# Optimization experiments

Hardware: AMD Instinct MI355X
Metric: run time of the kernel (lower is better)

Reference implementation:

```python
import jax, jax.numpy as jnp
import numpy as np

NUM_HEADS = 4   # forced by reshape(B, N, num_heads, C) of a dim*4 projection
BN_EPS = 1e-5


def _chamfer(a, b):
    # a, b: [B, N, 3] -> symmetric chamfer distance (mean of nearest sq-dists)
    d = (jnp.sum(a ** 2, -1)[:, :, None] + jnp.sum(b ** 2, -1)[:, None, :]
         - 2.0 * jnp.einsum('bnc,bmc->bnm', a, b))
    return jnp.mean(jnp.min(d, axis=2)) + jnp.mean(jnp.min(d, axis=1))


def _forward(xs, pc1, bn_gamma, bn_beta, q_w, kv_w, proj_w, proj_b, map_w, map_b):
    B, F, C, N = xs.shape
    H = NUM_HEADS
    scale = C ** -0.5  # head_dim == dim in this module (full-dim heads)

    def per_item(x):  # x: [F, C, N]
        # BatchNorm1d in eval mode (running_mean=0, running_var=1)
        xn = (x / jnp.sqrt(1.0 + BN_EPS)) * bn_gamma[:, None] + bn_beta[:, None]
        xn = xn.transpose(0, 2, 1)                 # [F, N, C]
        xr = xn[::-1]                              # flip over frame axis
        q = (xn @ q_w.T).reshape(F, N, H, C).transpose(0, 2, 1, 3)        # [F,H,N,C]
        kv = (xr @ kv_w.T).reshape(F, N, 2, H, C).transpose(2, 0, 3, 1, 4)
        k, v = kv[0], kv[1]                        # [F,H,N,C]
        attn = jax.nn.softmax(jnp.einsum('fhnc,fhmc->fhnm', q, k) * scale, axis=-1)
        o = jnp.einsum('fhnm,fhmc->fhnc', attn, v).transpose(0, 2, 1, 3)  # [F,N,H,C]
        xa = (o[0] + o[1]).transpose(1, 0, 2)      # [H, N, C]: sum of first two frames
        xa = xa @ proj_w.T + proj_b                # [H, N, C] x_appearance
        fr = xa @ map_w.T + map_b                  # [H, N, 3] frames (mapping_xyz)
        return xa, fr

    xa, frames = jax.vmap(per_item)(xs)            # [B,H,N,C], [B,H,N,3]
    pc1t = pc1.transpose(0, 2, 1)                  # [B, N, 3]
    loss = _chamfer(pc1t + frames[:, 0], pc1t)
    return xa[:, 1:], frames[:, 1:], loss


def setup_inputs() -> dict:
    key = jax.random.key(0)
    ks = jax.random.split(key, 8)
    B, F, C, N = 2, 4, 64, 2048
    return {
        'xs': jax.random.normal(ks[0], (B, F, C, N), jnp.float32),
        'pc1': jax.random.normal(ks[1], (B, 3, N), jnp.float32),
        'pc2': jax.random.normal(ks[2], (B, 3, N), jnp.float32),
        'bn_gamma': jnp.ones((C,), jnp.float32),
        'bn_beta': jnp.zeros((C,), jnp.float32),
        'q_w': 0.02 * jax.random.normal(ks[3], (4 * C, C), jnp.float32),
        'kv_w': 0.02 * jax.random.normal(ks[4], (8 * C, C), jnp.float32),
        'proj_w': 0.02 * jax.random.normal(ks[5], (C, C), jnp.float32),
        'proj_b': jnp.zeros((C,), jnp.float32),
        'map_w': 0.02 * jax.random.normal(ks[6], (3, C), jnp.float32),
        'map_b': jnp.zeros((3,), jnp.float32),
    }


def reference(xs, pc1, pc2, bn_gamma, bn_beta, q_w, kv_w, proj_w, proj_b, map_w, map_b):
    # pc2 is accepted by the torch forward but unused in its body
    return _forward(xs, pc1, bn_gamma, bn_beta, q_w, kv_w, proj_w, proj_b, map_w, map_b)
```

## Files before the change

### kernel.cpp

```cpp
#include <hip/hip_runtime.h>
#include <hip/hip_bf16.h>

#define NPTS 2048
#define LOG2E 1.4426950408889634f
#define NJC 16
#define JCH 128
#define KSPLIT 8

typedef short bf16x8 __attribute__((ext_vector_type(8)));
typedef float f32x4 __attribute__((ext_vector_type(4)));
typedef unsigned uint32x4 __attribute__((ext_vector_type(4)));
typedef __attribute__((address_space(3))) char lds_char;
typedef __attribute__((address_space(1))) const char glob_char;

union PBU { uint32x4 u; bf16x8 v; };

static __device__ __forceinline__ unsigned cvt_pk_bf16(float a, float b) {
    unsigned r;
    asm("v_cvt_pk_bf16_f32 %0, %1, %2" : "=v"(r) : "v"(a), "v"(b));
    return r;
}
static __device__ __forceinline__ float b2f(unsigned short u) {
    return __uint_as_float((unsigned)u << 16);
}

__global__ __launch_bounds__(256) void prep_all(const float* __restrict__ xs,
                                                const float* __restrict__ gamma,
                                                const float* __restrict__ beta,
                                                const float* __restrict__ q_w,
                                                const float* __restrict__ kv_w,
                                                const float* __restrict__ proj_w,
                                                __hip_bfloat16* __restrict__ xT,
                                                __hip_bfloat16* __restrict__ Wpb,
                                                __hip_bfloat16* __restrict__ Wb) {
    const int bid = blockIdx.x;
    const int t = threadIdx.x;
    if (bid < 256) {
        const int fr = bid >> 5;
        const int n0 = (bid & 31) * 64;
        const float* __restrict__ A = xs + (size_t)fr * 64 * NPTS;

        __shared__ float As[64][68];
        __shared__ float sg[64], sb[64];

        if (t < 64) {
            const float inv = 1.0f / sqrtf(1.0f + 1e-5f);
            sg[t] = gamma[t] * inv;
            sb[t] = beta[t];
        }
        const int tx = t & 15, ty = t >> 4;
        for (int r = 0; r < 4; ++r) {
            int row = ty + 16 * r, col = tx * 4;
            *(float4*)&As[row][col] = *(const float4*)&A[(size_t)row * NPTS + n0 + col];
        }
        __syncthreads();

        const int nl = t >> 2, c0 = (t & 3) * 16;
        bf16x8 v0, v1;
#pragma unroll
        for (int j = 0; j < 8; ++j) {
            float a = As[c0 + j][nl] * sg[c0 + j] + sb[c0 + j];
            v0[j] = (short)__bfloat16_as_ushort(__float2bfloat16(a));
        }
#pragma unroll
        for (int j = 0; j < 8; ++j) {
            float a = As[c0 + 8 + j][nl] * sg[c0 + 8 + j] + sb[c0 + 8 + j];
            v1[j] = (short)__bfloat16_as_ushort(__float2bfloat16(a));
        }
        __hip_bfloat16* dst = xT + ((size_t)fr * NPTS + n0 + nl) * 64 + c0;
        *(bf16x8*)(dst) = v0;
        *(bf16x8*)(dst + 8) = v1;
    } else {
        const int row = (bid - 256) * 256 + t;
        if (row < 768) {
            const float* src;
            float scale;
            if (row < 256) { src = q_w + row * 64;          scale = 0.125f * LOG2E; }
            else           { src = kv_w + (row - 256) * 64; scale = 1.0f; }
            for (int c = 0; c < 64; ++c)
                Wpb[row * 64 + c] = __float2bfloat16(src[c] * scale);
        } else if (row < 832) {
            const int j = row - 768;
            for (int c = 0; c < 64; ++c)
                Wb[j * 64 + c] = __float2bfloat16(proj_w[j * 64 + c]);
        }
    }
}

__global__ __launch_bounds__(256) void qkv_mfma(const __hip_bfloat16* __restrict__ xT,
                                                const __hip_bfloat16* __restrict__ Wpb,
                                                __hip_bfloat16* __restrict__ Qg,
                                                __hip_bfloat16* __restrict__ Kg,
                                                __hip_bfloat16* __restrict__ Vtg) {
    const int bf = blockIdx.z;
    const int b = bf >> 1, f01 = bf & 1;
    const int jt = blockIdx.y;
    const int f_src = (jt < 4) ? f01 : (3 - f01);
    const int n0 = blockIdx.x * 64;

    const int t = threadIdx.x, lane = t & 63, w = t >> 6;
    const int l15 = lane & 15, g = (lane >> 4) & 3;

    const __hip_bfloat16* __restrict__ xfb = xT + (size_t)(b * 4 + f_src) * NPTS * 64;

    if (jt < 8) {
        const __hip_bfloat16* wp = Wpb + (size_t)(jt * 64 + w * 16 + l15) * 64 + g * 8;
        bf16x8 wf0 = *(const bf16x8*)(wp);
        bf16x8 wf1 = *(const bf16x8*)(wp + 32);
        __hip_bfloat16* __restrict__ dst = (jt < 4 ? Qg : Kg) + (size_t)bf * NPTS * 256;
        const int jb = (jt & 3) * 64 + w * 16 + g * 4;
#pragma unroll
        for (int nt = 0; nt < 4; ++nt) {
            const __hip_bfloat16* xp = xfb + (size_t)(n0 + nt * 16 + l15) * 64 + g * 8;
            bf16x8 xf0 = *(const bf16x8*)(xp);
            bf16x8 xf1 = *(const bf16x8*)(xp + 32);
            f32x4 d = (f32x4){0.f, 0.f, 0.f, 0.f};
            d = __builtin_amdgcn_mfma_f32_16x16x32_bf16(wf0, xf0, d, 0, 0, 0);
            d = __builtin_amdgcn_mfma_f32_16x16x32_bf16(wf1, xf1, d, 0, 0, 0);
            uint2 pv;
            pv.x = cvt_pk_bf16(d[0], d[1]);
            pv.y = cvt_pk_bf16(d[2], d[3]);
            *(uint2*)&dst[(size_t)(n0 + nt * 16 + l15) * 256 + jb] = pv;
        }
    } else {
        const __hip_bfloat16* xp = xfb + (size_t)(n0 + w * 16 + l15) * 64 + g * 8;
        bf16x8 xf0 = *(const bf16x8*)(xp);
        bf16x8 xf1 = *(const bf16x8*)(xp + 32);
        __hip_bfloat16* __restrict__ dst = Vtg + (size_t)bf * 256 * NPTS;
#pragma unroll
        for (int tj = 0; tj < 4; ++tj) {
            const int ch = (jt - 8) * 64 + tj * 16 + l15;
            const __hip_bfloat16* wp = Wpb + (size_t)(512 + ch) * 64 + g * 8;
            bf16x8 wf0 = *(const bf16x8*)(wp);
            bf16x8 wf1 = *(const bf16x8*)(wp + 32);
            f32x4 d = (f32x4){0.f, 0.f, 0.f, 0.f};
            d = __builtin_amdgcn_mfma_f32_16x16x32_bf16(xf0, wf0, d, 0, 0, 0);
            d = __builtin_amdgcn_mfma_f32_16x16x32_bf16(xf1, wf1, d, 0, 0, 0);
            uint2 pv;
            pv.x = cvt_pk_bf16(d[0], d[1]);
            pv.y = cvt_pk_bf16(d[2], d[3]);
            *(uint2*)&dst[(size_t)ch * NPTS + n0 + w * 16 + g * 4] = pv;
        }
    }
}

__global__ __launch_bounds__(256, 4) void attn_mfma(const __hip_bfloat16* __restrict__ Qg,
                                                    const __hip_bfloat16* __restrict__ Kg,
                                                    const __hip_bfloat16* __restrict__ Vtg,
                                                    __hip_bfloat16* __restrict__ OTb,
                                                    float* __restrict__ Lp) {
    const int combo = blockIdx.x;
    const int bf = combo >> 2, h = combo & 3;
    const int n0 = blockIdx.y * 128;
    const int split = blockIdx.z;
    const int kbase = split * (NPTS / KSPLIT);
    const int NT = NPTS / KSPLIT / 32;

    __shared__ __align__(16) char smem[32768];

    const int t = threadIdx.x;
    const int lane = t & 63, w = t >> 6;
    const int l15 = lane & 15, g = (lane >> 4) & 3;

    const int krow = w * 8 + (lane >> 3), kslot = lane & 7;
    const int vrow = w * 16 + (lane >> 2), vslot = lane & 3;
    const int kcs = (kslot ^ (krow & 7)) * 8;
    const int vcs = (vslot ^ ((vrow >> 1) & 3)) * 8;

    const __hip_bfloat16* qbase =
        Qg + ((size_t)bf * NPTS + n0 + w * 32 + l15) * 256 + h * 64 + g * 8;
    bf16x8 qf[2][2];
    qf[0][0] = *(const bf16x8*)(qbase);
    qf[0][1] = *(const bf16x8*)(qbase + 32);
    qf[1][0] = *(const bf16x8*)(qbase + 16 * 256);
    qf[1][1] = *(const bf16x8*)(qbase + 16 * 256 + 32);

    const __hip_bfloat16* kgb = Kg + (size_t)bf * NPTS * 256 + h * 64;
    const __hip_bfloat16* vgb = Vtg + ((size_t)bf * 256 + h * 64) * NPTS;

    int koff[2][2], voff[4];
#pragma unroll
    for (int tt = 0; tt < 2; ++tt) {
        const int row = tt * 16 + l15;
#pragma unroll
        for (int s = 0; s < 2; ++s)
            koff[tt][s] = row * 128 + (((s * 4 + g) ^ (row & 7)) << 4);
    }
#pragma unroll
    for (int ct = 0; ct < 4; ++ct) {
        const int row = ct * 16 + l15;
        voff[ct] = 4096 + row * 64 + ((g ^ ((row >> 1) & 3)) << 4);
    }

    f32x4 oacc[2][4];
    float lsum[2] = {0.f, 0.f};
#pragma unroll
    for (int f = 0; f < 2; ++f)
#pragma unroll
        for (int r = 0; r < 4; ++r) oacc[f][r] = (f32x4){0.f, 0.f, 0.f, 0.f};

    auto stage = [&](int kt) {
        const int bsel = kt & 3;
        const __hip_bfloat16* ksrc = kgb + (size_t)(kbase + kt * 32 + krow) * 256 + kcs;
        __builtin_amdgcn_global_load_lds((const glob_char*)ksrc,
            (lds_char*)(smem + bsel * 8192 + w * 1024), 16, 0, 0);
        const __hip_bfloat16* vsrc = vgb + (size_t)vrow * NPTS + kbase + kt * 32 + vcs;
        __builtin_amdgcn_global_load_lds((const glob_char*)vsrc,
            (lds_char*)(smem + bsel * 8192 + 4096 + w * 1024), 16, 0, 0);
    };

    auto tile = [&](int kt) {
        const char* B = smem + (kt & 3) * 8192;
        bf16x8 kf[2][2];
#pragma unroll
        for (int tt = 0; tt < 2; ++tt)
#pragma unroll
            for (int s = 0; s < 2; ++s)
                kf[tt][s] = *(const bf16x8*)(B + koff[tt][s]);

        bf16x8 pb[2];
#pragma unroll
        for (int f = 0; f < 2; ++f) {
            f32x4 st0 = (f32x4){0.f, 0.f, 0.f, 0.f}, st1 = st0;
            st0 = __builtin_amdgcn_mfma_f32_16x16x32_bf16(kf[0][0], qf[f][0], st0, 0, 0, 0);
            st0 = __builtin_amdgcn_mfma_f32_16x16x32_bf16(kf[0][1], qf[f][1], st0, 0, 0, 0);
            st1 = __builtin_amdgcn_mfma_f32_16x16x32_bf16(kf[1][0], qf[f][0], st1, 0, 0, 0);
            st1 = __builtin_amdgcn_mfma_f32_16x16x32_bf16(kf[1][1], qf[f][1], st1, 0, 0, 0);
            float p00 = exp2f(st0[0]);
            float p01 = exp2f(st0[1]);
            float p02 = exp2f(st0[2]);
            float p03 = exp2f(st0[3]);
            float p10 = exp2f(st1[0]);
            float p11 = exp2f(st1[1]);
            float p12 = exp2f(st1[2]);
            float p13 = exp2f(st1[3]);
            lsum[f] += ((p00 + p01) + (p02 + p03)) + ((p10 + p11) + (p12 + p13));
            unsigned x0 = cvt_pk_bf16(p00, p01);
            unsigned x1 = cvt_pk_bf16(p02, p03);
            unsigned y0 = cvt_pk_bf16(p10, p11);
            unsigned y1 = cvt_pk_bf16(p12, p13);
            asm("v_permlane32_swap_b32 %0, %1" : "+v"(x0), "+v"(y0));
            asm("v_permlane16_swap_b32 %0, %1" : "+v"(x0), "+v"(y0));
            asm("v_permlane32_swap_b32 %0, %1" : "+v"(x1), "+v"(y1));
            asm("v_permlane16_swap_b32 %0, %1" : "+v"(x1), "+v"(y1));
            PBU pu;
            pu.u = (uint32x4){x0, x1, y0, y1};
            pb[f] = pu.v;
        }

#pragma unroll
        for (int ct = 0; ct < 4; ++ct) {
            bf16x8 vf = *(const bf16x8*)(B + voff[ct]);
            oacc[0][ct] = __builtin_amdgcn_mfma_f32_16x16x32_bf16(vf, pb[0], oacc[0][ct], 0, 0, 0);
            oacc[1][ct] = __builtin_amdgcn_mfma_f32_16x16x32_bf16(vf, pb[1], oacc[1][ct], 0, 0, 0);
        }
    };

    stage(0);
    stage(1);
    for (int kt = 0; kt < NT - 2; ++kt) {
        stage(kt + 2);
        asm volatile("s_waitcnt vmcnt(4)" ::: "memory");
        asm volatile("s_waitcnt lgkmcnt(0)" ::: "memory");
        __builtin_amdgcn_s_barrier();
        asm volatile("" ::: "memory");
        tile(kt);
    }
    asm volatile("s_waitcnt vmcnt(2)" ::: "memory");
    asm volatile("s_waitcnt lgkmcnt(0)" ::: "memory");
    __builtin_amdgcn_s_barrier();
    asm volatile("" ::: "memory");
    tile(NT - 2);
    asm volatile("s_waitcnt vmcnt(0)" ::: "memory");
    asm volatile("s_waitcnt lgkmcnt(0)" ::: "memory");
    __builtin_amdgcn_s_barrier();
    asm volatile("" ::: "memory");
    tile(NT - 1);

    float l0 = lsum[0], l1 = lsum[1];
    l0 += __shfl_xor(l0, 16);
    l0 += __shfl_xor(l0, 32);
    l1 += __shfl_xor(l1, 16);
    l1 += __shfl_xor(l1, 32);
    const int qq = n0 + w * 32 + l15;
    if (lane < 16) {
        Lp[(size_t)(split * 16 + combo) * NPTS + qq] = l0;
        Lp[(size_t)(split * 16 + combo) * NPTS + qq + 16] = l1;
    }

    __hip_bfloat16* __restrict__ Op = OTb + (size_t)(split * 16 + combo) * 64 * NPTS;
#pragma unroll
    for (int ct = 0; ct < 4; ++ct)
#pragma unroll
        for (int r = 0; r < 4; ++r) {
            Op[(size_t)(ct * 16 + g * 4 + r) * NPTS + qq] = __float2bfloat16(oacc[0][ct][r]);
            Op[(size_t)(ct * 16 + g * 4 + r) * NPTS + qq + 16] = __float2bfloat16(oacc[1][ct][r]);
        }
}

__global__ __launch_bounds__(256) void proj_frames(const __hip_bfloat16* __restrict__ OTb,
                                                   const float* __restrict__ Lp,
                                                   const __hip_bfloat16* __restrict__ Wb,
                                                   const float* __restrict__ proj_b,
                                                   const float* __restrict__ map_w,
                                                   const float* __restrict__ map_b,
                                                   float* __restrict__ out,
                                                   float* __restrict__ frames0) {
    const int bh = blockIdx.y, b = bh >> 2, h = bh & 3;
    const int n0 = blockIdx.x * 64;
    const int cf0 = (b * 2 + 0) * 4 + h;
    const int cf1 = (b * 2 + 1) * 4 + h;

    __shared__ __align__(16) unsigned short Xn[64][72];
    __shared__ float xaS[64][68];

    const int t = threadIdx.x;
    const int lane = t & 63, w = t >> 6;
    const int tx = t & 15, ty = t >> 4;
    const int l15 = lane & 15, g = (lane >> 4) & 3;
    const int nc = n0 + tx * 4;

    float4 L0 = make_float4(0.f, 0.f, 0.f, 0.f), L1 = L0;
#pragma unroll
    for (int s = 0; s < KSPLIT; ++s) {
        float4 a = *(const float4*)&Lp[(size_t)(s * 16 + cf0) * NPTS + nc];
        L0.x += a.x; L0.y += a.y; L0.z += a.z; L0.w += a.w;
        float4 c = *(const float4*)&Lp[(size_t)(s * 16 + cf1) * NPTS + nc];
        L1.x += c.x; L1.y += c.y; L1.z += c.z; L1.w += c.w;
    }
    float4 inv0 = make_float4(1.f / L0.x, 1.f / L0.y, 1.f / L0.z, 1.f / L0.w);
    float4 inv1 = make_float4(1.f / L1.x, 1.f / L1.y, 1.f / L1.z, 1.f / L1.w);

    for (int r = 0; r < 4; ++r) {
        int row = ty + 16 * r, col = tx * 4;
        float x0 = 0.f, x1 = 0.f, x2 = 0.f, x3 = 0.f;
        float y0 = 0.f, y1 = 0.f, y2 = 0.f, y3 = 0.f;
#pragma unroll
        for (int s = 0; s < KSPLIT; ++s) {
            ushort4 u0 = *(const ushort4*)&OTb[((size_t)(s * 16 + cf0) * 64 + row) * NPTS + n0 + col];
            ushort4 u1 = *(const ushort4*)&OTb[((size_t)(s * 16 + cf1) * 64 + row) * NPTS + n0 + col];
            x0 += b2f(u0.x); x1 += b2f(u0.y); x2 += b2f(u0.z); x3 += b2f(u0.w);
            y0 += b2f(u1.x); y1 += b2f(u1.y); y2 += b2f(u1.z); y3 += b2f(u1.w);
        }
        Xn[col + 0][row] = __bfloat16_as_ushort(__float2bfloat16(x0 * inv0.x + y0 * inv1.x));
        Xn[col + 1][row] = __bfloat16_as_ushort(__float2bfloat16(x1 * inv0.y + y1 * inv1.y));
        Xn[col + 2][row] = __bfloat16_as_ushort(__float2bfloat16(x2 * inv0.z + y2 * inv1.z));
        Xn[col + 3][row] = __bfloat16_as_ushort(__float2bfloat16(x3 * inv0.w + y3 * inv1.w));
    }
    __syncthreads();

    {
        const __hip_bfloat16* wp = Wb + (size_t)(w * 16 + l15) * 64 + g * 8;
        bf16x8 wf0 = *(const bf16x8*)(wp);
        bf16x8 wf1 = *(const bf16x8*)(wp + 32);
        float pbias[4];
#pragma unroll
        for (int r = 0; r < 4; ++r) pbias[r] = proj_b[w * 16 + g * 4 + r];
#pragma unroll
        for (int nt = 0; nt < 4; ++nt) {
            bf16x8 xf0 = *(const bf16x8*)&Xn[nt * 16 + l15][g * 8];
            bf16x8 xf1 = *(const bf16x8*)&Xn[nt * 16 + l15][g * 8 + 32];
            f32x4 d = (f32x4){0.f, 0.f, 0.f, 0.f};
            d = __builtin_amdgcn_mfma_f32_16x16x32_bf16(wf0, xf0, d, 0, 0, 0);
            d = __builtin_amdgcn_mfma_f32_16x16x32_bf16(wf1, xf1, d, 0, 0, 0);
            float4 v = make_float4(d[0] + pbias[0], d[1] + pbias[1],
                                   d[2] + pbias[2], d[3] + pbias[3]);
            *(float4*)&xaS[nt * 16 + l15][w * 16 + g * 4] = v;
        }
    }
    __syncthreads();

    if (h >= 1) {
        float* __restrict__ xa_out = out + (size_t)(b * 3 + h - 1) * NPTS * 64;
        for (int r = 0; r < 4; ++r) {
            int n = ty + 16 * r;
            float4 v = *(const float4*)&xaS[n][tx * 4];
            *(float4*)&xa_out[(size_t)(n0 + n) * 64 + tx * 4] = v;
        }
    }

    if (t < 192) {
        int r = t / 3, j = t % 3;
        float s = map_b[j];
        for (int c = 0; c < 64; ++c) s += xaS[r][c] * map_w[j * 64 + c];
        int n = n0 + r;
        if (h == 0) frames0[((size_t)b * NPTS + n) * 3 + j] = s;
        else        out[786432 + ((size_t)(b * 3 + h - 1) * NPTS + n) * 3 + j] = s;
    }
}

__global__ __launch_bounds__(256) void chamfer_partial(const float* __restrict__ pc1,
                                                       const float* __restrict__ frames0,
                                                       float* __restrict__ partial) {
    const int z = blockIdx.z;
    const int dir = z >> 1, b = z & 1;
    const int i = blockIdx.x * 256 + threadIdx.x;
    const int j0 = blockIdx.y * JCH;
    const float* __restrict__ px = pc1 + (size_t)b * 3 * NPTS;
    const float* __restrict__ fr = frames0 + (size_t)b * NPTS * 3;

    __shared__ float4 sj[JCH];
    if (threadIdx.x < JCH) {
        int jj = j0 + threadIdx.x;
        float bx = px[jj], by = px[NPTS + jj], bz = px[2 * NPTS + jj];
        if (dir == 1) { bx += fr[jj * 3]; by += fr[jj * 3 + 1]; bz += fr[jj * 3 + 2]; }
        sj[threadIdx.x] = make_float4(bx, by, bz, bx * bx + by * by + bz * bz);
    }
    float ax = px[i], ay = px[NPTS + i], az = px[2 * NPTS + i];
    if (dir == 0) { ax += fr[i * 3]; ay += fr[i * 3 + 1]; az += fr[i * 3 + 2]; }
    const float a2 = ax * ax + ay * ay + az * az;
    __syncthreads();

    float best = 1e30f;
#pragma unroll 4
    for (int k = 0; k < JCH; ++k) {
        float4 p = sj[k];
        float d = a2 + p.w - 2.0f * (ax * p.x + ay * p.y + az * p.z);
        best = fminf(best, d);
    }
    partial[((size_t)z * NJC + blockIdx.y) * NPTS + i] = best;
}

__global__ __launch_bounds__(256) void chamfer_minsum(const float* __restrict__ partial,
                                                      double* __restrict__ sums) {
    const int gid = blockIdx.x * 256 + threadIdx.x;
    const int z = gid >> 11, i = gid & 2047;
    float best = 1e30f;
#pragma unroll
    for (int c = 0; c < NJC; ++c)
        best = fminf(best, partial[((size_t)z * NJC + c) * NPTS + i]);
    __shared__ double sm[256];
    sm[threadIdx.x] = (double)best;
    __syncthreads();
    for (int off = 128; off > 0; off >>= 1) {
        if (threadIdx.x < off) sm[threadIdx.x] += sm[threadIdx.x + off];
        __syncthreads();
    }
    if (threadIdx.x == 0) sums[blockIdx.x] = sm[0];
}

__global__ void chamfer_final(const double* __restrict__ sums, float* __restrict__ loss_out) {
    if (threadIdx.x == 0) {
        double s = 0.0;
        for (int k = 0; k < 32; ++k) s += sums[k];
        loss_out[0] = (float)(s / 4096.0);
    }
}

extern "C" void kernel_launch(void* const* d_in, const int* in_sizes, int n_in,
                              void* d_out, int out_size, void* d_ws, size_t ws_size,
                              hipStream_t stream) {
    const float* xs     = (const float*)d_in[0];
    const float* pc1    = (const float*)d_in[1];
    const float* gamma  = (const float*)d_in[3];
    const float* beta   = (const float*)d_in[4];
    const float* q_w    = (const float*)d_in[5];
    const float* kv_w   = (const float*)d_in[6];
    const float* proj_w = (const float*)d_in[7];
    const float* proj_b = (const float*)d_in[8];
    const float* map_w  = (const float*)d_in[9];
    const float* map_b  = (const float*)d_in[10];
    float* out = (float*)d_out;

    char* ws = (char*)d_ws;
    __hip_bfloat16* Qg  = (__hip_bfloat16*)(ws);
    __hip_bfloat16* Kg  = (__hip_bfloat16*)(ws + 4194304);
    __hip_bfloat16* Vtg = (__hip_bfloat16*)(ws + 8388608);
    __hip_bfloat16* OTb = (__hip_bfloat16*)(ws + 12582912);
    __hip_bfloat16* Wpb = (__hip_bfloat16*)(ws + 46137344);
    __hip_bfloat16* xT  = (__hip_bfloat16*)(ws + 46235648);
    float* frames0 = (float*)(ws + 48332800);
    float* partial = (float*)(ws + 48381952);
    double* sums   = (double*)(ws + 48906240);
    float* Lp      = (float*)(ws + 48906496);
    __hip_bfloat16* Wb  = (__hip_bfloat16*)(ws + 49955072);

    hipLaunchKernelGGL(prep_all, dim3(260), dim3(256), 0, stream,
                       xs, gamma, beta, q_w, kv_w, proj_w, xT, Wpb, Wb);
    hipLaunchKernelGGL(qkv_mfma, dim3(32, 12, 4), dim3(256), 0, stream,
                       xT, Wpb, Qg, Kg, Vtg);
    hipLaunchKernelGGL(attn_mfma, dim3(16, 16, KSPLIT), dim3(256), 0, stream,
                       Qg, Kg, Vtg, OTb, Lp);
    hipLaunchKernelGGL(proj_frames, dim3(32, 8), dim3(256), 0, stream,
                       OTb, Lp, Wb, proj_b, map_w, map_b, out, frames0);
    hipLaunchKernelGGL(chamfer_partial, dim3(NPTS / 256, NJC, 4), dim3(256), 0, stream,
                       pc1, frames0, partial);
    hipLaunchKernelGGL(chamfer_minsum, dim3(32), dim3(256), 0, stream,
                       partial, sums);
    hipLaunchKernelGGL(chamfer_final, dim3(1), dim3(64), 0, stream,
                       sums, out + 823296);
}
```

Measured before the change: 75.06 us.

## Fuse chamfer final reduction via atomic counter, add MFMA priority, drop lgkm waits

Removes the single-thread chamfer_final launch by having the last block of chamfer_minsum perform the final sum, using an atomic counter that prep_all resets. The attention kernel raises wave priority around MFMA groups with s_setprio. It also drops the explicit lgkmcnt(0) waits before the barriers in the attention pipeline. Removing those waits relies on the global_load_lds staging being covered by vmcnt alone, which could risk reading LDS data that has not landed yet.

```diff
diff --git a/kernel.cpp b/kernel.cpp
--- a/kernel.cpp
+++ b/kernel.cpp
@@ -32,7 +32,8 @@
                                                 const float* __restrict__ proj_w,
                                                 __hip_bfloat16* __restrict__ xT,
                                                 __hip_bfloat16* __restrict__ Wpb,
-                                                __hip_bfloat16* __restrict__ Wb) {
+                                                __hip_bfloat16* __restrict__ Wb,
+                                                unsigned* __restrict__ counter) {
     const int bid = blockIdx.x;
     const int t = threadIdx.x;
     if (bid < 256) {
@@ -83,6 +84,8 @@
             const int j = row - 768;
             for (int c = 0; c < 64; ++c)
                 Wb[j * 64 + c] = __float2bfloat16(proj_w[j * 64 + c]);
+        } else if (row == 1023) {
+            *counter = 0;
         }
     }
 }
@@ -222,10 +225,12 @@
 #pragma unroll
         for (int f = 0; f < 2; ++f) {
             f32x4 st0 = (f32x4){0.f, 0.f, 0.f, 0.f}, st1 = st0;
+            __builtin_amdgcn_s_setprio(1);
             st0 = __builtin_amdgcn_mfma_f32_16x16x32_bf16(kf[0][0], qf[f][0], st0, 0, 0, 0);
             st0 = __builtin_amdgcn_mfma_f32_16x16x32_bf16(kf[0][1], qf[f][1], st0, 0, 0, 0);
             st1 = __builtin_amdgcn_mfma_f32_16x16x32_bf16(kf[1][0], qf[f][0], st1, 0, 0, 0);
             st1 = __builtin_amdgcn_mfma_f32_16x16x32_bf16(kf[1][1], qf[f][1], st1, 0, 0, 0);
+            __builtin_amdgcn_s_setprio(0);
             float p00 = exp2f(st0[0]);
             float p01 = exp2f(st0[1]);
             float p02 = exp2f(st0[2]);
@@ -248,12 +253,14 @@
             pb[f] = pu.v;
         }
 
+        __builtin_amdgcn_s_setprio(1);
 #pragma unroll
         for (int ct = 0; ct < 4; ++ct) {
             bf16x8 vf = *(const bf16x8*)(B + voff[ct]);
             oacc[0][ct] = __builtin_amdgcn_mfma_f32_16x16x32_bf16(vf, pb[0], oacc[0][ct], 0, 0, 0);
             oacc[1][ct] = __builtin_amdgcn_mfma_f32_16x16x32_bf16(vf, pb[1], oacc[1][ct], 0, 0, 0);
         }
+        __builtin_amdgcn_s_setprio(0);
     };
 
     stage(0);
@@ -261,18 +268,15 @@
     for (int kt = 0; kt < NT - 2; ++kt) {
         stage(kt + 2);
         asm volatile("s_waitcnt vmcnt(4)" ::: "memory");
-        asm volatile("s_waitcnt lgkmcnt(0)" ::: "memory");
         __builtin_amdgcn_s_barrier();
         asm volatile("" ::: "memory");
         tile(kt);
     }
     asm volatile("s_waitcnt vmcnt(2)" ::: "memory");
-    asm volatile("s_waitcnt lgkmcnt(0)" ::: "memory");
     __builtin_amdgcn_s_barrier();
     asm volatile("" ::: "memory");
     tile(NT - 2);
     asm volatile("s_waitcnt vmcnt(0)" ::: "memory");
-    asm volatile("s_waitcnt lgkmcnt(0)" ::: "memory");
     __builtin_amdgcn_s_barrier();
     asm volatile("" ::: "memory");
     tile(NT - 1);
@@ -422,7 +426,9 @@
 }
 
 __global__ __launch_bounds__(256) void chamfer_minsum(const float* __restrict__ partial,
-                                                      double* __restrict__ sums) {
+                                                      double* __restrict__ sums,
+                                                      unsigned* __restrict__ counter,
+                                                      float* __restrict__ loss_out) {
     const int gid = blockIdx.x * 256 + threadIdx.x;
     const int z = gid >> 11, i = gid & 2047;
     float best = 1e30f;
@@ -436,14 +442,17 @@
         if (threadIdx.x < off) sm[threadIdx.x] += sm[threadIdx.x + off];
         __syncthreads();
     }
-    if (threadIdx.x == 0) sums[blockIdx.x] = sm[0];
-}
-
-__global__ void chamfer_final(const double* __restrict__ sums, float* __restrict__ loss_out) {
     if (threadIdx.x == 0) {
-        double s = 0.0;
-        for (int k = 0; k < 32; ++k) s += sums[k];
-        loss_out[0] = (float)(s / 4096.0);
+        sums[blockIdx.x] = sm[0];
+        __threadfence();
+        unsigned prev = atomicAdd(counter, 1u);
+        if (prev == 31u) {
+            __threadfence();
+            double s = 0.0;
+            for (int k = 0; k < 32; ++k) s += sums[k];
+            loss_out[0] = (float)(s / 4096.0);
+            *counter = 0;
+        }
     }
 }
 
@@ -474,9 +483,10 @@
     double* sums   = (double*)(ws + 48906240);
     float* Lp      = (float*)(ws + 48906496);
     __hip_bfloat16* Wb  = (__hip_bfloat16*)(ws + 49955072);
+    unsigned* counter   = (unsigned*)(ws + 49963264);
 
     hipLaunchKernelGGL(prep_all, dim3(260), dim3(256), 0, stream,
-                       xs, gamma, beta, q_w, kv_w, proj_w, xT, Wpb, Wb);
+                       xs, gamma, beta, q_w, kv_w, proj_w, xT, Wpb, Wb, counter);
     hipLaunchKernelGGL(qkv_mfma, dim3(32, 12, 4), dim3(256), 0, stream,
                        xT, Wpb, Qg, Kg, Vtg);
     hipLaunchKernelGGL(attn_mfma, dim3(16, 16, KSPLIT), dim3(256), 0, stream,
@@ -486,7 +496,5 @@
     hipLaunchKernelGGL(chamfer_partial, dim3(NPTS / 256, NJC, 4), dim3(256), 0, stream,
                        pc1, frames0, partial);
     hipLaunchKernelGGL(chamfer_minsum, dim3(32), dim3(256), 0, stream,
-                       partial, sums);
-    hipLaunchKernelGGL(chamfer_final, dim3(1), dim3(64), 0, stream,
-                       sums, out + 823296);
-}
+                       partial, sums, counter, out + 823296);
+}
```

New measurement: 75.01 us. Within noise of the previous version (-0.1%).
